# Performance work log

Measured on AMD Instinct MI355X. Metric: run time of the kernel, lower is better.

Reference implementation:

```python
import jax, jax.numpy as jnp
import numpy as np

U, I, D = 2048, 4096, 64


def setup_inputs() -> dict:
    key = jax.random.key(0)
    ks = jax.random.split(key, 16)
    s = 0.02  # weight scale (xavier-ish)
    inp = {
        "ui_input_mp": jax.random.uniform(ks[0], (U, I), jnp.float32),
        "ui_input_pmp": jax.random.uniform(ks[1], (U, I), jnp.float32),
        "Wu_mp": jax.random.normal(ks[2], (D, I), jnp.float32) * s,
        "Wu_pmp": jax.random.normal(ks[3], (D, I), jnp.float32) * s,
        "Wi_mp": jax.random.normal(ks[4], (D, U), jnp.float32) * s,
        "Wi_pmp": jax.random.normal(ks[5], (D, U), jnp.float32) * s,
        "mw_mp": jax.random.normal(ks[6], (I, D), jnp.float32) * s,
        "mb_mp": jnp.zeros((I,), jnp.float32),
        "aw_mp": jax.random.normal(ks[7], (I, I), jnp.float32) * s,
        "ab_mp": jnp.zeros((I,), jnp.float32),
        "Wat_mp": jax.random.normal(ks[8], (U, U + I), jnp.float32) * s,
        "mw_pmp": jax.random.normal(ks[9], (I, D), jnp.float32) * s,
        "mb_pmp": jnp.zeros((I,), jnp.float32),
        "aw_pmp": jax.random.normal(ks[10], (I, I), jnp.float32) * s,
        "ab_pmp": jnp.zeros((I,), jnp.float32),
        "Wat_pmp": jax.random.normal(ks[11], (U, U + I), jnp.float32) * s,
        "mlp_w": jax.random.normal(ks[12], (D, 2 * D), jnp.float32) * s,
        "mlp_b": jnp.zeros((D,), jnp.float32),
        "tr_w": jax.random.normal(ks[13], (D, D), jnp.float32) * s,
        "tr_b": jnp.zeros((D,), jnp.float32),
    }
    return inp


def _attention_weights(x, mw, mb, aw, ab, Wat):
    # x: [U+I, D]; mlp Linear(D,I)+ReLU (dropout=0), then tanh
    h = jnp.tanh(jax.nn.relu(x @ mw.T + mb))          # [U+I, I]
    a = jnp.tanh(h @ aw.T + ab)                        # [U+I, I]
    scores = Wat @ a                                   # [U, I]
    return jax.nn.softmax(scores, axis=1)


def _branch(ui, Wu, Wi, mw, mb, aw, ab, Wat):
    ue = ui @ Wu.T                                     # [U, D] user embeds
    ie = ui.T @ Wi.T                                   # [I, D] item embeds
    x = jnp.concatenate([ue, ie], axis=0)              # [U+I, D]
    at = _attention_weights(x, mw, mb, aw, ab, Wat)    # [U, I]
    ue_at = at @ ie                                    # [U, D]
    return ue, ie, ue_at


def reference(ui_input_mp, ui_input_pmp, Wu_mp, Wu_pmp, Wi_mp, Wi_pmp,
              mw_mp, mb_mp, aw_mp, ab_mp, Wat_mp,
              mw_pmp, mb_pmp, aw_pmp, ab_pmp, Wat_pmp,
              mlp_w, mlp_b, tr_w, tr_b):
    mlp = lambda z: jax.nn.sigmoid(z @ mlp_w.T + mlp_b)

    ue_mp, ie_mp, ue_mp_at = _branch(ui_input_mp, Wu_mp, Wi_mp,
                                     mw_mp, mb_mp, aw_mp, ab_mp, Wat_mp)
    ue_pmp, ie_pmp, ue_pmp_at = _branch(ui_input_pmp, Wu_pmp, Wi_pmp,
                                        mw_pmp, mb_pmp, aw_pmp, ab_pmp, Wat_pmp)

    u_mp = mlp(jnp.concatenate([ue_mp, ue_mp_at], axis=1))      # [U, D]
    u_pmp = mlp(jnp.concatenate([ue_pmp, ue_pmp_at], axis=1))   # [U, D]

    rate = jax.nn.sigmoid(u_mp + u_pmp)
    user_fusion = rate * u_mp + (1.0 - rate) * u_pmp            # [U, D]

    item_embeddings = mlp(jnp.concatenate([ie_mp, ie_pmp], axis=1))  # [I, D]

    user_embeds = jnp.tanh(user_fusion @ tr_w.T + tr_b)          # [U, D]
    return user_embeds, item_embeddings
```

## Files before the change

kernel.cpp:

```cpp
#include <hip/hip_runtime.h>
#include <stdint.h>
#include <math.h>


typedef short short8 __attribute__((ext_vector_type(8)));
typedef unsigned short ushort8 __attribute__((ext_vector_type(8)));
typedef unsigned char uchar8 __attribute__((ext_vector_type(8)));
typedef float f32x4 __attribute__((ext_vector_type(4)));
typedef int int4v __attribute__((ext_vector_type(4)));
typedef int int8v __attribute__((ext_vector_type(8)));

#define DEVI static __device__ __forceinline__

DEVI unsigned short f2bf(float f) {
  uint32_t u = __builtin_bit_cast(uint32_t, f);
  return (unsigned short)((u + 0x7fffu + ((u >> 16) & 1u)) >> 16);
}
DEVI unsigned char f2fp8(float f) {
  uint32_t u = __builtin_bit_cast(uint32_t, f);
  uint32_t s = (u >> 24) & 0x80u;
  uint32_t a = u & 0x7fffffffu;
  if (a >= 0x43e00000u) return (unsigned char)(s | 0x7eu);
  if (a < 0x3c800000u) {
    float af = __builtin_bit_cast(float, a);
    uint32_t n = (uint32_t)__builtin_rintf(af * 512.0f);
    return (unsigned char)(s | n);
  }
  uint32_t r = a + 0xfffffu + ((a >> 20) & 1u);
  return (unsigned char)(s | ((r >> 20) - 960u));
}
DEVI float sigmoidf_(float x) { return 1.0f / (1.0f + expf(-x)); }

DEVI void gld16(const void* g, void* l) {
  __builtin_amdgcn_global_load_lds(
      (const __attribute__((address_space(1))) unsigned int*)g,
      (__attribute__((address_space(3))) unsigned int*)l, 16, 0, 0);
}

#define MFMA16B(a, b, c) __builtin_amdgcn_mfma_f32_16x16x32_bf16(a, b, c, 0, 0, 0)
#define MFMAMX(a, b, c)                                              \
  __builtin_amdgcn_mfma_scale_f32_16x16x128_f8f6f4(                  \
      a, b, c, 0, 0, 0, 0x7f7f7f7fu, 0, 0x7f7f7f7fu)

__global__ __launch_bounds__(256) void k_f32_to_bf16(
    const float* __restrict__ s, unsigned short* __restrict__ d, long n) {
  long i0 = ((long)blockIdx.x * 256 + threadIdx.x) * 8;
  long stride = (long)gridDim.x * 256 * 8;
  for (long i = i0; i < n; i += stride) {
    f32x4 a = *(const f32x4*)(s + i);
    f32x4 b = *(const f32x4*)(s + i + 4);
    ushort8 o;
    o[0] = f2bf(a[0]); o[1] = f2bf(a[1]); o[2] = f2bf(a[2]); o[3] = f2bf(a[3]);
    o[4] = f2bf(b[0]); o[5] = f2bf(b[1]); o[6] = f2bf(b[2]); o[7] = f2bf(b[3]);
    *(ushort8*)(d + i) = o;
  }
}

__global__ __launch_bounds__(256) void k_f32_to_fp8(
    const float* __restrict__ s, unsigned char* __restrict__ d, long n,
    float scale) {
  long i0 = ((long)blockIdx.x * 256 + threadIdx.x) * 8;
  long stride = (long)gridDim.x * 256 * 8;
  for (long i = i0; i < n; i += stride) {
    f32x4 a = *(const f32x4*)(s + i);
    f32x4 b = *(const f32x4*)(s + i + 4);
    uchar8 o;
    o[0] = f2fp8(a[0] * scale); o[1] = f2fp8(a[1] * scale);
    o[2] = f2fp8(a[2] * scale); o[3] = f2fp8(a[3] * scale);
    o[4] = f2fp8(b[0] * scale); o[5] = f2fp8(b[1] * scale);
    o[6] = f2fp8(b[2] * scale); o[7] = f2fp8(b[3] * scale);
    *(uchar8*)(d + i) = o;
  }
}

template <int EPI>
__global__ __launch_bounds__(512, 1) void k_gemmMX(
    const unsigned char* __restrict__ A0, const unsigned char* __restrict__ A1,
    const unsigned char* __restrict__ B0, const unsigned char* __restrict__ B1,
    float* __restrict__ outF, unsigned char* __restrict__ oB0,
    unsigned char* __restrict__ oB1, const float* __restrict__ bias0,
    const float* __restrict__ bias1, int M, int N, int K, long zsf,
    float dsc) {
  const int gx = gridDim.x;
  const int nwg = gx * gridDim.y;
  const int flat = blockIdx.y * gx + blockIdx.x;
  const int swz = (flat & 7) * (nwg >> 3) + (flat >> 3);
  const int bxi = swz % gx, byi = swz / gx;

  const int bz = blockIdx.z;
  const unsigned char* A = bz ? A1 : A0;
  const unsigned char* B = bz ? B1 : B0;
  unsigned char* outB = bz ? oB1 : oB0;
  const float* bias = bz ? bias1 : bias0;

  __shared__ unsigned char lds[131072];
  const int tid = threadIdx.x, lane = tid & 63;
  const int wid = tid >> 6, wr = wid >> 2, wc = wid & 3;
  const int bm = bxi * 256, bn = byi * 256;
  const int rl = lane & 15, q = lane >> 4;

  const int x7 = rl & 7;
  const int c0 = ((2 * q) ^ x7) << 4;
  const int c1 = ((2 * q + 1) ^ x7) << 4;

  const unsigned char* gA = A + (size_t)bm * K;
  const unsigned char* gB = B + (size_t)bn * K;

  auto stage = [&](int kc, int bufb) {
#pragma unroll
    for (int i = 0; i < 4; i++) {
      const int cid = tid + 512 * i;
      const int r = cid >> 3;
      const int go = r * K + (((cid & 7) ^ (r & 7)) << 4) + kc;
      const int dst = cid << 4;
      gld16(gA + go, &lds[bufb + dst]);
      gld16(gB + go, &lds[bufb + 32768 + dst]);
    }
  };

  f32x4 acc[8][4] = {};

  auto frag = [&](const unsigned char* p) {
    int4v lo = *(const int4v*)(p + c0);
    int4v hi = *(const int4v*)(p + c1);
    return __builtin_shufflevector(lo, hi, 0, 1, 2, 3, 4, 5, 6, 7);
  };

  auto body = [&](int kc, int cb, int pb) {
    if (kc + 128 < K) stage(kc + 128, pb);

    const unsigned char* As = lds + cb + wr * 16384;
    const unsigned char* Bs = lds + cb + 32768 + wc * 8192;

    int8v bf[4];
#pragma unroll
    for (int nf = 0; nf < 4; nf++) bf[nf] = frag(Bs + (nf * 16 + rl) * 128);

    __builtin_amdgcn_s_setprio(1);
#pragma unroll
    for (int mi = 0; mi < 8; mi++) {
      int8v a = frag(As + (mi * 16 + rl) * 128);
#pragma unroll
      for (int nf = 0; nf < 4; nf++)
        acc[mi][nf] = MFMAMX(a, bf[nf], acc[mi][nf]);
    }
    __builtin_amdgcn_s_setprio(0);

    if (kc + 128 < K) {
      asm volatile("s_waitcnt vmcnt(0)\ns_barrier" ::: "memory");
    }
  };

  stage(0, 0);
  asm volatile("s_waitcnt vmcnt(0)\ns_barrier" ::: "memory");

  for (int k0 = 0; k0 < K; k0 += 256) {
    body(k0, 0, 65536);
    body(k0 + 128, 65536, 0);
  }

#pragma unroll
  for (int m = 0; m < 8; m++) {
#pragma unroll
    for (int nf = 0; nf < 4; nf++) {
      const int col = bn + wc * 64 + nf * 16 + rl;
#pragma unroll
      for (int r = 0; r < 4; r++) {
        const int row = bm + wr * 128 + m * 16 + q * 4 + r;
        const float v = acc[m][nf][r] * dsc;
        if (EPI == 0)
          outF[(long)bz * zsf + (size_t)row * N + col] = v;
        else
          outB[(size_t)row * N + col] = f2fp8(tanhf(v + bias[row]));
      }
    }
  }
}

__global__ __launch_bounds__(256) void k_gemmH(
    const unsigned short* __restrict__ A0, const unsigned short* __restrict__ A1,
    const unsigned short* __restrict__ B0, const unsigned short* __restrict__ B1,
    unsigned char* __restrict__ o0, unsigned char* __restrict__ o1,
    const float* __restrict__ bias0, const float* __restrict__ bias1, int M,
    int N, int K) {
  const int bz = blockIdx.z;
  const unsigned short* A = bz ? A1 : A0;
  const unsigned short* B = bz ? B1 : B0;
  unsigned char* out8 = bz ? o1 : o0;
  const float* bias = bz ? bias1 : bias0;

  __shared__ unsigned short As[128 * 32];
  __shared__ unsigned short Bs[128 * 32];
  const int tid = threadIdx.x, lane = tid & 63, wid = tid >> 6;
  const int wr = wid >> 1, wc = wid & 1;
  const int bm = blockIdx.x * 128, bn = blockIdx.y * 128;
  const int c0 = tid, c1 = tid + 256;
  const int s0 = ((c0 & 3) ^ ((c0 >> 3) & 3)) << 3;
  const int s1 = ((c1 & 3) ^ ((c1 >> 3) & 3)) << 3;
  const int rl = lane & 15, q = lane >> 4;
  const int qe = (q ^ ((rl >> 1) & 3)) << 3;

  f32x4 acc[4][4] = {};

  for (int k0 = 0; k0 < K; k0 += 32) {
    gld16(A + (size_t)(bm + (c0 >> 2)) * K + k0 + s0, As + c0 * 8);
    gld16(A + (size_t)(bm + (c1 >> 2)) * K + k0 + s1, As + c1 * 8);
    gld16(B + (size_t)(bn + (c0 >> 2)) * K + k0 + s0, Bs + c0 * 8);
    gld16(B + (size_t)(bn + (c1 >> 2)) * K + k0 + s1, Bs + c1 * 8);
    __syncthreads();

    short8 af[4], bfr[4];
#pragma unroll
    for (int mi = 0; mi < 4; mi++)
      af[mi] = *(const short8*)(As + (wr * 64 + mi * 16 + rl) * 32 + qe);
#pragma unroll
    for (int ni = 0; ni < 4; ni++)
      bfr[ni] = *(const short8*)(Bs + (wc * 64 + ni * 16 + rl) * 32 + qe);
#pragma unroll
    for (int mi = 0; mi < 4; mi++)
#pragma unroll
      for (int ni = 0; ni < 4; ni++)
        acc[mi][ni] = MFMA16B(af[mi], bfr[ni], acc[mi][ni]);
    __syncthreads();
  }

#pragma unroll
  for (int mi = 0; mi < 4; mi++) {
#pragma unroll
    for (int ni = 0; ni < 4; ni++) {
      const int col = bn + wc * 64 + ni * 16 + rl;
#pragma unroll
      for (int r = 0; r < 4; r++) {
        const int row = bm + wr * 64 + mi * 16 + q * 4 + r;
        out8[(size_t)row * N + col] =
            f2fp8(tanhf(fmaxf(acc[mi][ni][r] + bias[col], 0.0f)));
      }
    }
  }
}

template <int AMODE, int BMODE>
__global__ __launch_bounds__(256) void k_sgemm64s(
    const void* __restrict__ A0, const void* __restrict__ A1,
    const void* __restrict__ B0, const void* __restrict__ B1,
    float* __restrict__ P, int kchunk, int lda, int ldb, int M) {
  const int br = blockIdx.z, kz = blockIdx.y, KS = gridDim.y;
  const void* Av = br ? A1 : A0;
  const void* Bv = br ? B1 : B0;

  __shared__ unsigned short As[64 * 40];
  __shared__ unsigned short Bs[64 * 40];
  const int tid = threadIdx.x, lane = tid & 63, w = tid >> 6;
  const int tm = blockIdx.x * 64;

  f32x4 acc[4] = {};
  const int kbeg = kz * kchunk, kend = kbeg + kchunk;

  for (int k0 = kbeg; k0 < kend; k0 += 32) {
    if (AMODE == 0) {
      const float* Af = (const float*)Av;
      const int m = tid >> 2, k8 = (tid & 3) << 3;
      f32x4 x0 = *(const f32x4*)(Af + (size_t)(tm + m) * lda + k0 + k8);
      f32x4 x1 = *(const f32x4*)(Af + (size_t)(tm + m) * lda + k0 + k8 + 4);
      ushort8 o;
      o[0] = f2bf(x0[0]); o[1] = f2bf(x0[1]); o[2] = f2bf(x0[2]); o[3] = f2bf(x0[3]);
      o[4] = f2bf(x1[0]); o[5] = f2bf(x1[1]); o[6] = f2bf(x1[2]); o[7] = f2bf(x1[3]);
      *(ushort8*)(As + m * 40 + k8) = o;
    } else if (AMODE == 1) {
      const float* Af = (const float*)Av;
#pragma unroll
      for (int t = 0; t < 2; t++) {
        const int c = tid + t * 256;
        const int u = c >> 4, i4 = (c & 15) << 2;
        f32x4 x = *(const f32x4*)(Af + (size_t)(k0 + u) * lda + tm + i4);
        As[(i4 + 0) * 40 + u] = f2bf(x[0]);
        As[(i4 + 1) * 40 + u] = f2bf(x[1]);
        As[(i4 + 2) * 40 + u] = f2bf(x[2]);
        As[(i4 + 3) * 40 + u] = f2bf(x[3]);
      }
    } else {
      const unsigned short* Ab = (const unsigned short*)Av;
      const int m = tid >> 2, k8 = (tid & 3) << 3;
      *(ushort8*)(As + m * 40 + k8) =
          *(const ushort8*)(Ab + (size_t)(tm + m) * lda + k0 + k8);
    }
    if (BMODE == 0) {
      const float* Bf = (const float*)Bv;
      const int n = tid >> 2, k8 = (tid & 3) << 3;
      f32x4 x0 = *(const f32x4*)(Bf + (size_t)n * ldb + k0 + k8);
      f32x4 x1 = *(const f32x4*)(Bf + (size_t)n * ldb + k0 + k8 + 4);
      ushort8 o;
      o[0] = f2bf(x0[0]); o[1] = f2bf(x0[1]); o[2] = f2bf(x0[2]); o[3] = f2bf(x0[3]);
      o[4] = f2bf(x1[0]); o[5] = f2bf(x1[1]); o[6] = f2bf(x1[2]); o[7] = f2bf(x1[3]);
      *(ushort8*)(Bs + n * 40 + k8) = o;
    } else {
      const unsigned short* Bb = (const unsigned short*)Bv;
      const int n = tid >> 2, k8 = (tid & 3) << 3;
      *(ushort8*)(Bs + n * 40 + k8) =
          *(const ushort8*)(Bb + (size_t)n * ldb + k0 + k8);
    }
    __syncthreads();

    const int kr = (lane >> 4) << 3;
    short8 a = *(const short8*)(As + (w * 16 + (lane & 15)) * 40 + kr);
#pragma unroll
    for (int ni = 0; ni < 4; ni++) {
      short8 bb = *(const short8*)(Bs + (ni * 16 + (lane & 15)) * 40 + kr);
      acc[ni] = MFMA16B(a, bb, acc[ni]);
    }
    __syncthreads();
  }

  float* out = P + ((size_t)(br * KS + kz) * M) * 64;
#pragma unroll
  for (int ni = 0; ni < 4; ni++) {
    const int col = ni * 16 + (lane & 15);
#pragma unroll
    for (int r = 0; r < 4; r++) {
      const int row = tm + w * 16 + ((lane >> 4) << 2) + r;
      out[(size_t)row * 64 + col] = acc[ni][r];
    }
  }
}

template <int WF, int WB, int WT>
__global__ __launch_bounds__(256) void k_reduce(
    const float* __restrict__ P, size_t pbr_stride, float* F0, float* F1,
    unsigned short* Bo0, unsigned short* Bo1, unsigned short* T0,
    unsigned short* T1, int M, int KS, int ldT) {
  const int br = blockIdx.y;
  const float* Pp = P + (size_t)br * pbr_stride;
  const size_t i = (size_t)blockIdx.x * 256 + threadIdx.x;
  const size_t n = (size_t)M * 64;
  float s = 0.f;
  for (int k = 0; k < KS; k++) s += Pp[(size_t)k * n + i];
  if (WF) (br ? F1 : F0)[i] = s;
  if (WB) (br ? Bo1 : Bo0)[i] = f2bf(s);
  if (WT) {
    const int row = (int)(i >> 6), col = (int)(i & 63);
    (br ? T1 : T0)[(size_t)col * ldT + row] = f2bf(s);
  }
}

__global__ __launch_bounds__(256) void k_softmax(
    const float* __restrict__ S, unsigned short* __restrict__ P0,
    unsigned short* __restrict__ P1, long slab) {
  const int row = blockIdx.x, br = blockIdx.y, tid = threadIdx.x;
  const float* s = S + (size_t)br * slab + (size_t)row * 4096;
  float v[16];
  float m = -1e30f;
#pragma unroll
  for (int j = 0; j < 16; j++) {
    v[j] = s[tid + j * 256];
    m = fmaxf(m, v[j]);
  }
  __shared__ float red[4], red2[4];
  for (int o = 32; o; o >>= 1) m = fmaxf(m, __shfl_down(m, o));
  if ((tid & 63) == 0) red[tid >> 6] = m;
  __syncthreads();
  m = fmaxf(fmaxf(red[0], red[1]), fmaxf(red[2], red[3]));
  float sum = 0.0f;
#pragma unroll
  for (int j = 0; j < 16; j++) {
    v[j] = expf(v[j] - m);
    sum += v[j];
  }
  for (int o = 32; o; o >>= 1) sum += __shfl_down(sum, o);
  if ((tid & 63) == 0) red2[tid >> 6] = sum;
  __syncthreads();
  const float inv = 1.0f / (red2[0] + red2[1] + red2[2] + red2[3]);
  unsigned short* p = (br ? P1 : P0) + (size_t)row * 4096;
#pragma unroll
  for (int j = 0; j < 16; j++) p[tid + j * 256] = f2bf(v[j] * inv);
}

__global__ __launch_bounds__(256) void k_user(
    const float* __restrict__ ue_mp, const float* __restrict__ ueat_mp,
    const float* __restrict__ ue_pmp, const float* __restrict__ ueat_pmp,
    const float* __restrict__ mlp_w, const float* __restrict__ mlp_b,
    const float* __restrict__ tr_w, const float* __restrict__ tr_b,
    float* __restrict__ out) {
  const int tid = threadIdx.x, d = tid & 63, w = tid >> 6;
  const int m = blockIdx.x * 4 + w;
  __shared__ float fus[4][64];
  float a1 = mlp_b[d], a2 = a1;
  const float* r1 = ue_mp + (size_t)m * 64;
  const float* r2 = ueat_mp + (size_t)m * 64;
  const float* r3 = ue_pmp + (size_t)m * 64;
  const float* r4 = ueat_pmp + (size_t)m * 64;
  const float* w1 = mlp_w + (size_t)d * 128;
#pragma unroll 8
  for (int k = 0; k < 64; k++) {
    const float wv = w1[k];
    a1 += r1[k] * wv;
    a2 += r3[k] * wv;
  }
#pragma unroll 8
  for (int k = 0; k < 64; k++) {
    const float wv = w1[64 + k];
    a1 += r2[k] * wv;
    a2 += r4[k] * wv;
  }
  const float u1 = sigmoidf_(a1), u2 = sigmoidf_(a2);
  const float rate = sigmoidf_(u1 + u2);
  fus[w][d] = rate * u1 + (1.0f - rate) * u2;
  __syncthreads();
  float o = tr_b[d];
  const float* tw = tr_w + (size_t)d * 64;
#pragma unroll 8
  for (int k = 0; k < 64; k++) o += fus[w][k] * tw[k];
  out[(size_t)m * 64 + d] = tanhf(o);
}

__global__ __launch_bounds__(256) void k_item(
    const float* __restrict__ ie_mp, const float* __restrict__ ie_pmp,
    const float* __restrict__ mlp_w, const float* __restrict__ mlp_b,
    float* __restrict__ out) {
  const int tid = threadIdx.x, d = tid & 63, w = tid >> 6;
  const int i = blockIdx.x * 4 + w;
  float a = mlp_b[d];
  const float* r1 = ie_mp + (size_t)i * 64;
  const float* r2 = ie_pmp + (size_t)i * 64;
  const float* wp = mlp_w + (size_t)d * 128;
#pragma unroll 8
  for (int k = 0; k < 64; k++) {
    a += r1[k] * wp[k];
    a += r2[k] * wp[64 + k];
  }
  out[(size_t)i * 64 + d] = sigmoidf_(a);
}

extern "C" void kernel_launch(void* const* d_in, const int* in_sizes, int n_in,
                              void* d_out, int out_size, void* d_ws,
                              size_t ws_size, hipStream_t stream) {
  const int U = 2048, I = 4096, D = 64, UI = 6144;
  const float WSC = 16.0f, DSC = 1.0f / 16.0f;

  const float* ui[2] = {(const float*)d_in[0], (const float*)d_in[1]};
  const float* Wu[2] = {(const float*)d_in[2], (const float*)d_in[3]};
  const float* Wi[2] = {(const float*)d_in[4], (const float*)d_in[5]};
  const float* mw[2] = {(const float*)d_in[6], (const float*)d_in[11]};
  const float* mb[2] = {(const float*)d_in[7], (const float*)d_in[12]};
  const float* aw[2] = {(const float*)d_in[8], (const float*)d_in[13]};
  const float* ab[2] = {(const float*)d_in[9], (const float*)d_in[14]};
  const float* Wat[2] = {(const float*)d_in[10], (const float*)d_in[15]};
  const float* mlp_w = (const float*)d_in[16];
  const float* mlp_b = (const float*)d_in[17];
  const float* tr_w = (const float*)d_in[18];
  const float* tr_b = (const float*)d_in[19];

  char* ws = (char*)d_ws;
  size_t off = 0;
  auto alloc = [&](size_t bytes) {
    void* p = ws + off;
    off += (bytes + 255) & ~(size_t)255;
    return p;
  };
  unsigned char* aw_f8[2] = {(unsigned char*)alloc((size_t)I * I),
                             (unsigned char*)alloc((size_t)I * I)};
  unsigned short* mw_bf[2] = {(unsigned short*)alloc((size_t)I * D * 2),
                              (unsigned short*)alloc((size_t)I * D * 2)};
  unsigned char* h_f8[2] = {(unsigned char*)alloc((size_t)UI * I),
                            (unsigned char*)alloc((size_t)UI * I)};
  unsigned char* aT_f8[2] = {(unsigned char*)alloc((size_t)I * UI),
                             (unsigned char*)alloc((size_t)I * UI)};
  float* scores = (float*)alloc((size_t)U * I * 4 * 2);
  unsigned short* at_bf[2] = {(unsigned short*)alloc((size_t)U * I * 2),
                              (unsigned short*)alloc((size_t)U * I * 2)};
  unsigned short* x_bf[2];
  float* ue_f[2];
  float* ie_f[2];
  unsigned short* ieT[2];
  float* ueat_f[2];
  for (int b = 0; b < 2; b++) {
    x_bf[b] = (unsigned short*)alloc((size_t)UI * D * 2);
    ue_f[b] = (float*)alloc((size_t)U * D * 4);
    ie_f[b] = (float*)alloc((size_t)I * D * 4);
    ieT[b] = (unsigned short*)alloc((size_t)D * I * 2);
    ueat_f[b] = (float*)alloc((size_t)U * D * 4);
  }
  float* pue = (float*)h_f8[0];
  float* pie = (float*)aT_f8[0];
  float* pueat = scores;
  unsigned char* Wat_f8[2] = {(unsigned char*)at_bf[0],
                              (unsigned char*)at_bf[1]};
  const long zsf = (long)U * I;

  const dim3 blk(256);

  k_sgemm64s<0, 0><<<dim3(U / 64, 8, 2), blk, 0, stream>>>(
      ui[0], ui[1], Wu[0], Wu[1], pue, I / 8, I, I, U);
  k_reduce<1, 1, 0><<<dim3(U * 64 / 256, 2), blk, 0, stream>>>(
      pue, (size_t)8 * U * 64, ue_f[0], ue_f[1], x_bf[0], x_bf[1], nullptr,
      nullptr, U, 8, 0);
  k_sgemm64s<1, 0><<<dim3(I / 64, 8, 2), blk, 0, stream>>>(
      ui[0], ui[1], Wi[0], Wi[1], pie, U / 8, I, U, I);
  k_reduce<1, 1, 1><<<dim3(I * 64 / 256, 2), blk, 0, stream>>>(
      pie, (size_t)8 * I * 64, ie_f[0], ie_f[1], x_bf[0] + (size_t)U * D,
      x_bf[1] + (size_t)U * D, ieT[0], ieT[1], I, 8, I);

  for (int b = 0; b < 2; b++) {
    k_f32_to_fp8<<<2048, blk, 0, stream>>>(aw[b], aw_f8[b], (long)I * I, WSC);
    k_f32_to_fp8<<<2048, blk, 0, stream>>>(Wat[b], Wat_f8[b], (long)U * UI, WSC);
    k_f32_to_bf16<<<128, blk, 0, stream>>>(mw[b], mw_bf[b], (long)I * D);
  }

  k_gemmH<<<dim3(UI / 128, I / 128, 2), blk, 0, stream>>>(
      x_bf[0], x_bf[1], mw_bf[0], mw_bf[1], h_f8[0], h_f8[1], mb[0], mb[1],
      UI, I, D);

  k_gemmMX<1><<<dim3(I / 256, UI / 256, 2), dim3(512), 0, stream>>>(
      aw_f8[0], aw_f8[1], h_f8[0], h_f8[1], nullptr, aT_f8[0], aT_f8[1],
      ab[0], ab[1], I, UI, I, 0, DSC);

  k_gemmMX<0><<<dim3(U / 256, I / 256, 2), dim3(512), 0, stream>>>(
      Wat_f8[0], Wat_f8[1], aT_f8[0], aT_f8[1], scores, nullptr, nullptr,
      nullptr, nullptr, U, I, UI, zsf, DSC);

  k_softmax<<<dim3(U, 2), blk, 0, stream>>>(scores, at_bf[0], at_bf[1], zsf);

  k_sgemm64s<2, 2><<<dim3(U / 64, 8, 2), blk, 0, stream>>>(
      at_bf[0], at_bf[1], ieT[0], ieT[1], pueat, I / 8, I, I, U);
  k_reduce<1, 0, 0><<<dim3(U * 64 / 256, 2), blk, 0, stream>>>(
      pueat, (size_t)8 * U * 64, ueat_f[0], ueat_f[1], nullptr, nullptr,
      nullptr, nullptr, U, 8, 0);

  float* out_user = (float*)d_out;
  float* out_item = (float*)d_out + (size_t)U * D;
  k_user<<<U / 4, blk, 0, stream>>>(ue_f[0], ueat_f[0], ue_f[1], ueat_f[1],
                                    mlp_w, mlp_b, tr_w, tr_b, out_user);
  k_item<<<I / 4, blk, 0, stream>>>(ie_f[0], ie_f[1], mlp_w, mlp_b, out_item);
}
```

Baseline: 602.0 us.

## Shrink MX fp8 GEMM tile to 256x128 single-buffered for higher occupancy

The fp8 MX GEMM tile drops from 256x256 to 256x128, with 8 waves arranged 4x2 and half the accumulators per wave. The LDS double buffer (128KB) becomes a single 48KB buffer with a plain load, wait, compute loop, and launch bounds rise to allow up to 4 blocks per CU. The goal is to hide global-load latency through more resident workgroups instead of in-block prefetch. In exchange, data reuse per tile is lower, there is no software pipelining inside a block, and each k-step now needs two barriers.

```diff
diff --git a/kernel.cpp b/kernel.cpp
--- a/kernel.cpp
+++ b/kernel.cpp
@@ -73,8 +73,10 @@
   }
 }
 
+struct I4Pair { int4v lo, hi; };
+
 template <int EPI>
-__global__ __launch_bounds__(512, 1) void k_gemmMX(
+__global__ __launch_bounds__(512, 4) void k_gemmMX(
     const unsigned char* __restrict__ A0, const unsigned char* __restrict__ A1,
     const unsigned char* __restrict__ B0, const unsigned char* __restrict__ B1,
     float* __restrict__ outF, unsigned char* __restrict__ oB0,
@@ -93,10 +95,10 @@
   unsigned char* outB = bz ? oB1 : oB0;
   const float* bias = bz ? bias1 : bias0;
 
-  __shared__ unsigned char lds[131072];
+  __shared__ unsigned char lds[49152];
   const int tid = threadIdx.x, lane = tid & 63;
-  const int wid = tid >> 6, wr = wid >> 2, wc = wid & 3;
-  const int bm = bxi * 256, bn = byi * 256;
+  const int wid = tid >> 6, wr = wid >> 1, wc = wid & 1;
+  const int bm = bxi * 256, bn = byi * 128;
   const int rl = lane & 15, q = lane >> 4;
 
   const int x7 = rl & 7;
@@ -106,67 +108,64 @@
   const unsigned char* gA = A + (size_t)bm * K;
   const unsigned char* gB = B + (size_t)bn * K;
 
-  auto stage = [&](int kc, int bufb) {
+  auto stage = [&](int kc) {
 #pragma unroll
     for (int i = 0; i < 4; i++) {
       const int cid = tid + 512 * i;
       const int r = cid >> 3;
       const int go = r * K + (((cid & 7) ^ (r & 7)) << 4) + kc;
-      const int dst = cid << 4;
-      gld16(gA + go, &lds[bufb + dst]);
-      gld16(gB + go, &lds[bufb + 32768 + dst]);
+      gld16(gA + go, &lds[cid << 4]);
+    }
+#pragma unroll
+    for (int i = 4; i < 6; i++) {
+      const int cid = tid + 512 * i;
+      const int r = (cid - 2048) >> 3;
+      const int go = r * K + (((cid & 7) ^ (r & 7)) << 4) + kc;
+      gld16(gB + go, &lds[cid << 4]);
     }
   };
 
-  f32x4 acc[8][4] = {};
+  f32x4 acc[4][4] = {};
 
   auto frag = [&](const unsigned char* p) {
-    int4v lo = *(const int4v*)(p + c0);
-    int4v hi = *(const int4v*)(p + c1);
-    return __builtin_shufflevector(lo, hi, 0, 1, 2, 3, 4, 5, 6, 7);
+    I4Pair t;
+    t.lo = *(const int4v*)(p + c0);
+    t.hi = *(const int4v*)(p + c1);
+    return __builtin_bit_cast(int8v, t);
   };
 
-  auto body = [&](int kc, int cb, int pb) {
-    if (kc + 128 < K) stage(kc + 128, pb);
-
-    const unsigned char* As = lds + cb + wr * 16384;
-    const unsigned char* Bs = lds + cb + 32768 + wc * 8192;
+  for (int k0 = 0; k0 < K; k0 += 128) {
+    stage(k0);
+    asm volatile("s_waitcnt vmcnt(0)\ns_barrier" ::: "memory");
 
     int8v bf[4];
 #pragma unroll
-    for (int nf = 0; nf < 4; nf++) bf[nf] = frag(Bs + (nf * 16 + rl) * 128);
+    for (int nf = 0; nf < 4; nf++)
+      bf[nf] = frag(lds + 32768 + (wc * 64 + nf * 16 + rl) * 128);
 
     __builtin_amdgcn_s_setprio(1);
 #pragma unroll
-    for (int mi = 0; mi < 8; mi++) {
-      int8v a = frag(As + (mi * 16 + rl) * 128);
+    for (int mi = 0; mi < 4; mi++) {
+      int8v a = frag(lds + (wr * 64 + mi * 16 + rl) * 128);
 #pragma unroll
       for (int nf = 0; nf < 4; nf++)
         acc[mi][nf] = MFMAMX(a, bf[nf], acc[mi][nf]);
     }
     __builtin_amdgcn_s_setprio(0);
 
-    if (kc + 128 < K) {
-      asm volatile("s_waitcnt vmcnt(0)\ns_barrier" ::: "memory");
-    }
-  };
-
-  stage(0, 0);
-  asm volatile("s_waitcnt vmcnt(0)\ns_barrier" ::: "memory");
-
-  for (int k0 = 0; k0 < K; k0 += 256) {
-    body(k0, 0, 65536);
-    body(k0 + 128, 65536, 0);
-  }
-
-#pragma unroll
-  for (int m = 0; m < 8; m++) {
+    if (k0 + 128 < K) {
+      asm volatile("s_barrier" ::: "memory");
+    }
+  }
+
+#pragma unroll
+  for (int m = 0; m < 4; m++) {
 #pragma unroll
     for (int nf = 0; nf < 4; nf++) {
       const int col = bn + wc * 64 + nf * 16 + rl;
 #pragma unroll
       for (int r = 0; r < 4; r++) {
-        const int row = bm + wr * 128 + m * 16 + q * 4 + r;
+        const int row = bm + wr * 64 + m * 16 + q * 4 + r;
         const float v = acc[m][nf][r] * dsc;
         if (EPI == 0)
           outF[(long)bz * zsf + (size_t)row * N + col] = v;
@@ -509,11 +508,11 @@
       x_bf[0], x_bf[1], mw_bf[0], mw_bf[1], h_f8[0], h_f8[1], mb[0], mb[1],
       UI, I, D);
 
-  k_gemmMX<1><<<dim3(I / 256, UI / 256, 2), dim3(512), 0, stream>>>(
+  k_gemmMX<1><<<dim3(I / 256, UI / 128, 2), dim3(512), 0, stream>>>(
       aw_f8[0], aw_f8[1], h_f8[0], h_f8[1], nullptr, aT_f8[0], aT_f8[1],
       ab[0], ab[1], I, UI, I, 0, DSC);
 
-  k_gemmMX<0><<<dim3(U / 256, I / 256, 2), dim3(512), 0, stream>>>(
+  k_gemmMX<0><<<dim3(U / 256, I / 128, 2), dim3(512), 0, stream>>>(
       Wat_f8[0], Wat_f8[1], aT_f8[0], aT_f8[1], scores, nullptr, nullptr,
       nullptr, nullptr, U, I, UI, zsf, DSC);
 
```

New measurement: 575.7 us (median of 2 runs). -4.4%, faster.
